# Performance work log

Hardware: AMD Instinct MI355X
Metric: run time of the kernel (lower is better)

Reference implementation:

```python
import jax, jax.numpy as jnp
import numpy as np

G = 29      # grid_size
D = 15      # displacement_width
R = 0.4     # disp_range
C = 16      # feature channels
S = 48      # feature spatial size
D3 = D ** 3


def _axis_coords(n, scale=1.0):
    # torch affine_grid (align_corners=False) coords: -1 + (2i+1)/n
    i = jnp.arange(n, dtype=jnp.float32)
    return scale * ((2.0 * i + 1.0) / n - 1.0)


def _make_grid(n, scale=1.0):
    # affine_grid flatten order is (d,h,w) with last dim (x,y,z)
    c = _axis_coords(n, scale)
    zz, yy, xx = jnp.meshgrid(c, c, c, indexing='ij')
    return jnp.stack([xx, yy, zz], axis=-1).reshape(-1, 3)  # [n^3, 3]


def _tri_sample(feat, pts):
    # feat [C,Dz,Hy,Wx]; pts [N,3] normalized (x,y,z); border-clamped trilinear
    Cc, Dz, Hy, Wx = feat.shape
    def unnorm(c, n):
        return jnp.clip(((c + 1.0) * n - 1.0) * 0.5, 0.0, n - 1.0)
    px = unnorm(pts[:, 0], Wx)
    py = unnorm(pts[:, 1], Hy)
    pz = unnorm(pts[:, 2], Dz)
    x0f, y0f, z0f = jnp.floor(px), jnp.floor(py), jnp.floor(pz)
    wx, wy, wz = px - x0f, py - y0f, pz - z0f
    x0 = x0f.astype(jnp.int32); y0 = y0f.astype(jnp.int32); z0 = z0f.astype(jnp.int32)
    x1 = jnp.minimum(x0 + 1, Wx - 1)
    y1 = jnp.minimum(y0 + 1, Hy - 1)
    z1 = jnp.minimum(z0 + 1, Dz - 1)
    flat = feat.reshape(Cc, -1)
    def g(zi, yi, xi):
        return flat[:, (zi * Hy + yi) * Wx + xi]  # [C,N]
    return (g(z0, y0, x0) * ((1 - wz) * (1 - wy) * (1 - wx))
          + g(z0, y0, x1) * ((1 - wz) * (1 - wy) * wx)
          + g(z0, y1, x0) * ((1 - wz) * wy * (1 - wx))
          + g(z0, y1, x1) * ((1 - wz) * wy * wx)
          + g(z1, y0, x0) * (wz * (1 - wy) * (1 - wx))
          + g(z1, y0, x1) * (wz * (1 - wy) * wx)
          + g(z1, y1, x0) * (wz * wy * (1 - wx))
          + g(z1, y1, x1) * (wz * wy * wx))


def _avg3(x):  # 3x3x3 avg pool, stride 1, VALID, over last 3 dims of [N,a,b,c]
    s = jax.lax.reduce_window(x, 0.0, jax.lax.add, (1, 3, 3, 3), (1, 1, 1, 1), 'VALID')
    return s / 27.0


def _min3(x):  # 3x3x3 min pool == -maxpool(-x)
    return jax.lax.reduce_window(x, float('inf'), jax.lax.min, (1, 3, 3, 3), (1, 1, 1, 1), 'VALID')


def _pad_rep(x, p):  # ReplicationPad3d over last 3 dims
    return jnp.pad(x, ((0, 0), (p, p), (p, p), (p, p)), mode='edge')


def _minavg_disp(x):  # pad1 -> min3 -> avg3 -> avg3  (size preserved)
    return _avg3(_avg3(_min3(_pad_rep(x, 3))))


def _avg_grid(x):  # pad2 -> avg3 -> avg3 (size preserved)
    return _avg3(_avg3(_pad_rep(x, 2)))


def setup_inputs() -> dict:
    key = jax.random.key(0)
    k1, k2 = jax.random.split(key)
    feat00 = jax.random.normal(k1, (1, C, S, S, S), dtype=jnp.float32)
    feat50 = jax.random.normal(k2, (1, C, S, S, S), dtype=jnp.float32)
    alpha = jnp.array([1.0, 0.1, 1.0, 1.0, 0.1, 1.0], dtype=jnp.float32)
    return {"feat00": feat00, "feat50": feat50, "alpha": alpha}


def reference(feat00, feat50, alpha):
    grid = _make_grid(G)        # [G^3,3]
    shift = _make_grid(D, R)    # [D^3,3]
    f0 = feat00[0]
    f5 = feat50[0]

    def slab(g):  # g [G^2,3] -> cost [G^2, D^3]
        pts = (g[:, None, :] + shift[None, :, :]).reshape(-1, 3)
        mov = _tri_sample(f5, pts).reshape(C, G * G, D3)
        fix = _tri_sample(f0, g)[:, :, None]            # [C,G^2,1]
        d = fix - mov
        return alpha[1] + alpha[0] * jnp.sum(d * d, axis=0)

    # scan over G slabs (as the torch loop does) to bound memory
    dc = jax.lax.map(jax.checkpoint(slab), grid.reshape(G, G * G, 3))
    dc = dc.reshape(G ** 3, D, D, D)                    # deeds_cost

    def disp_to_grid(x):
        return x.reshape(G ** 3, D3).T.reshape(D3, G, G, G)

    def grid_to_disp(x):
        return x.reshape(D3, G ** 3).T.reshape(G ** 3, D, D, D)

    c = _minavg_disp(dc)
    ca = grid_to_disp(_avg_grid(disp_to_grid(c)))
    c = alpha[4] + alpha[2] * dc + alpha[3] * ca
    c = _minavg_disp(c)
    ca2 = _avg_grid(disp_to_grid(c)).reshape(D3, G ** 3).T   # [G^3, D^3]
    cost_soft = jax.nn.softmax(-alpha[5] * ca2, axis=1)
    pred_xyz = cost_soft @ shift                              # [G^3, 3]
    return cost_soft, pred_xyz
```

## Files before the change

### kernel.cpp

```cpp
#include <hip/hip_runtime.h>
#include <cstdint>

#define GG   29
#define GG2  841
#define GG3  24389
#define DD   15
#define DD3  3375
#define SS   48
#define CC   16
#define NVOX (SS*SS*SS)
#define FT_ELEMS (NVOX*CC)
#define WXY  20
#define WZC  6
#define WELE4 (WXY*WXY*WZC)

#define MW0 (1.0f/9.0f)
#define MW1 (2.0f/9.0f)
#define MW2 (3.0f/9.0f)

__device__ __forceinline__ int clampi(int v, int lo, int hi) {
    return min(max(v, lo), hi);
}

__device__ __forceinline__ float4 f4min3(float4 a, float4 b, float4 c) {
    return make_float4(fminf(fminf(a.x,b.x),c.x), fminf(fminf(a.y,b.y),c.y),
                       fminf(fminf(a.z,b.z),c.z), fminf(fminf(a.w,b.w),c.w));
}
__device__ __forceinline__ void f4acc(float4& o, float w, float4 a) {
    o.x += w*a.x; o.y += w*a.y; o.z += w*a.z; o.w += w*a.w;
}

__global__ void __launch_bounds__(256) k_transpose4(const float* __restrict__ f,
                                                    float* __restrict__ ft) {
    int v = blockIdx.x * 256 + threadIdx.x;
    int cg4 = blockIdx.y;
    float4 o = make_float4(f[(4*cg4+0)*NVOX + v], f[(4*cg4+1)*NVOX + v],
                           f[(4*cg4+2)*NVOX + v], f[(4*cg4+3)*NVOX + v]);
    ((float4*)ft)[(size_t)cg4 * NVOX + v] = o;
}

template<int JZ0, int NJZ>
__device__ __forceinline__ void cost_chunk(const float4* __restrict__ f5f4,
                                           float4* win, const float4* fixs4,
                                           int tid, float pzb, int xb, int yb,
                                           int orel, float wx, float wy,
                                           bool active, float (&acc)[15]) {
    float pz0 = fminf(fmaxf(pzb + 1.28f * (float)JZ0, 0.0f), 47.0f);
    int zb = min((int)floorf(pz0), SS - WZC);
    int   z0r[NJZ];
    float wzs[NJZ];
    #pragma unroll
    for (int k = 0; k < NJZ; ++k) {
        float pz = fminf(fmaxf(pzb + 1.28f * (float)(JZ0 + k), 0.0f), 47.0f);
        int z0 = min((int)floorf(pz), 46);
        z0r[k] = z0 - zb;
        wzs[k] = pz - (float)z0;
    }

    int vox[10];
    #pragma unroll
    for (int k = 0; k < 10; ++k) {
        int idx = tid + (k << 8);
        if (idx < WELE4) {
            int lz  = idx / 400;
            int rem = idx - lz * 400;
            int ly  = rem / 20;
            int lx  = rem - ly * 20;
            vox[k] = ((zb + lz) * SS + (yb + ly)) * SS + (xb + lx);
        }
    }

    auto bilin = [&](int zr) -> float4 {
        const float4* P = win + zr * 400 + orel;
        float4 a = P[0], b = P[1], c = P[20], d = P[21];
        float r0x = a.x + wx*(b.x-a.x), r0y = a.y + wx*(b.y-a.y);
        float r0z = a.z + wx*(b.z-a.z), r0w = a.w + wx*(b.w-a.w);
        float r1x = c.x + wx*(d.x-c.x), r1y = c.y + wx*(d.y-c.y);
        float r1z = c.z + wx*(d.z-c.z), r1w = c.w + wx*(d.w-c.w);
        return make_float4(r0x + wy*(r1x-r0x), r0y + wy*(r1y-r0y),
                           r0z + wy*(r1z-r0z), r0w + wy*(r1w-r0w));
    };

    #pragma unroll 1
    for (int cg4 = 0; cg4 < 4; ++cg4) {
        const float4* src = f5f4 + (size_t)cg4 * NVOX;
        #pragma unroll
        for (int k = 0; k < 10; ++k) {
            int idx = tid + (k << 8);
            if (idx < WELE4) win[idx] = src[vox[k]];
        }
        __syncthreads();

        if (active) {
            float4 fx = fixs4[cg4];
            float4 pA = make_float4(0.f,0.f,0.f,0.f), pB = pA;
            int zprev = -99;
            #pragma unroll
            for (int k = 0; k < NJZ; ++k) {
                int zr = z0r[k]; float wz = wzs[k];
                if (zr != zprev) {
                    if (zr == zprev + 1) pA = pB;
                    else                 pA = bilin(zr);
                    pB = bilin(zr + 1);
                    zprev = zr;
                }
                float mx = pA.x + wz*(pB.x-pA.x);
                float my = pA.y + wz*(pB.y-pA.y);
                float mz = pA.z + wz*(pB.z-pA.z);
                float mw = pA.w + wz*(pB.w-pA.w);
                float dx = fx.x - mx, dy = fx.y - my, dz = fx.z - mz, dw = fx.w - mw;
                acc[JZ0 + k] += dx*dx + dy*dy + dz*dz + dw*dw;
            }
        }
        __syncthreads();
    }
}

__global__ void __launch_bounds__(256, 4) k_cost4(const float* __restrict__ f5t,
                                                  const float* __restrict__ feat00,
                                                  const float* __restrict__ alpha,
                                                  float* __restrict__ dc) {
    __shared__ float4 win[WELE4];
    __shared__ float4 fixs4[4];

    int tid = threadIdx.x;
    int g = blockIdx.x;
    int gx = g % GG; int gy = (g / GG) % GG; int gz = g / GG2;

    if (tid < CC) {
        int giv[3] = {gx, gy, gz};
        int i0[3]; float w[3];
        #pragma unroll
        for (int a = 0; a < 3; ++a) {
            float cgv = (2.0f * giv[a] + 1.0f) / 29.0f - 1.0f;
            float p = ((cgv + 1.0f) * 48.0f - 1.0f) * 0.5f;
            p = fminf(fmaxf(p, 0.0f), 47.0f);
            float fl = floorf(p);
            i0[a] = (int)fl; w[a] = p - fl;
        }
        int x0 = i0[0], y0 = i0[1], z0 = i0[2];
        int x1 = min(x0 + 1, 47), y1 = min(y0 + 1, 47), z1 = min(z0 + 1, 47);
        float wx = w[0], wy = w[1], wz = w[2];
        float ux = 1.0f - wx, uy = 1.0f - wy, uz = 1.0f - wz;
        const float* fc = feat00 + (size_t)tid * NVOX;
        int zy00 = (z0 * SS + y0) * SS, zy01 = (z0 * SS + y1) * SS;
        int zy10 = (z1 * SS + y0) * SS, zy11 = (z1 * SS + y1) * SS;
        ((float*)fixs4)[tid] =
              uz*uy*ux * fc[zy00 + x0] + uz*uy*wx * fc[zy00 + x1]
            + uz*wy*ux * fc[zy01 + x0] + uz*wy*wx * fc[zy01 + x1]
            + wz*uy*ux * fc[zy10 + x0] + wz*uy*wx * fc[zy10 + x1]
            + wz*wy*ux * fc[zy11 + x0] + wz*wy*wx * fc[zy11 + x1];
    }

    float pxb = 24.0f * (float)(2 * gx + 1) / 29.0f - 9.46f;
    float pyb = 24.0f * (float)(2 * gy + 1) / 29.0f - 9.46f;
    float pzb = 24.0f * (float)(2 * gz + 1) / 29.0f - 9.46f;
    int xb = min((int)floorf(fminf(fmaxf(pxb, 0.0f), 47.0f)), SS - WXY);
    int yb = min((int)floorf(fminf(fmaxf(pyb, 0.0f), 47.0f)), SS - WXY);

    bool active = tid < 225;
    int jx = tid % 15, jy = tid / 15;
    float px = fminf(fmaxf(pxb + 1.28f * (float)jx, 0.0f), 47.0f);
    float py = fminf(fmaxf(pyb + 1.28f * (float)jy, 0.0f), 47.0f);
    int x0 = min((int)floorf(px), 46);
    int y0 = min((int)floorf(py), 46);
    float wx = px - (float)x0;
    float wy = py - (float)y0;
    int orel = (y0 - yb) * WXY + (x0 - xb);

    float acc[15];
    #pragma unroll
    for (int k = 0; k < 15; ++k) acc[k] = 0.0f;

    const float4* f5f4 = (const float4*)f5t;
    cost_chunk<0, 4>(f5f4, win, fixs4, tid, pzb, xb, yb, orel, wx, wy, active, acc);
    cost_chunk<4, 4>(f5f4, win, fixs4, tid, pzb, xb, yb, orel, wx, wy, active, acc);
    cost_chunk<8, 4>(f5f4, win, fixs4, tid, pzb, xb, yb, orel, wx, wy, active, acc);
    cost_chunk<12,3>(f5f4, win, fixs4, tid, pzb, xb, yb, orel, wx, wy, active, acc);

    float a0 = alpha[0], a1 = alpha[1];
    if (active) {
        float* dcrow = dc + (size_t)g * DD3;
        #pragma unroll
        for (int k = 0; k < 15; ++k) dcrow[k * 225 + tid] = a1 + a0 * acc[k];
    }
}

__device__ __forceinline__ void minavg_cols(float* U, float* V, float (&v)[15],
                                            int tid, float* __restrict__ outrow) {
    if (tid < 225) {
        float m[20];
        #pragma unroll
        for (int zi = 0; zi < 20; ++zi)
            m[zi] = fminf(fminf(v[clampi(zi-3,0,14)], v[clampi(zi-2,0,14)]),
                          v[clampi(zi-1,0,14)]);
        float4* u4 = (float4*)&U[tid*20];
        const float4* m4 = (const float4*)m;
        #pragma unroll
        for (int q = 0; q < 5; ++q) u4[q] = m4[q];
    }
    __syncthreads();
    for (int c = tid; c < 285; c += 256) {
        int sx = c % 15, yi = c / 15;
        const float4* A = (const float4*)&U[(clampi(yi-3,0,14)*15 + sx)*20];
        const float4* B = (const float4*)&U[(clampi(yi-2,0,14)*15 + sx)*20];
        const float4* Cc= (const float4*)&U[(clampi(yi-1,0,14)*15 + sx)*20];
        float4* vv = (float4*)&V[c*20];
        #pragma unroll
        for (int q = 0; q < 5; ++q) vv[q] = f4min3(A[q], B[q], Cc[q]);
    }
    __syncthreads();
    for (int c = tid; c < 361; c += 256) {
        int xi = c % 19, yi = c / 19;
        int s0 = clampi(xi-3,0,14), s1 = clampi(xi-2,0,14), s2 = clampi(xi-1,0,14);
        const float4* A = (const float4*)&V[(yi*15 + s0)*20];
        const float4* B = (const float4*)&V[(yi*15 + s1)*20];
        const float4* Cc= (const float4*)&V[(yi*15 + s2)*20];
        float m[20];
        float4* m4 = (float4*)m;
        #pragma unroll
        for (int q = 0; q < 5; ++q) m4[q] = f4min3(A[q], B[q], Cc[q]);
        float cz[16];
        #pragma unroll
        for (int zi = 0; zi < 15; ++zi)
            cz[zi] = MW0*(m[zi] + m[zi+4]) + MW1*(m[zi+1] + m[zi+3]) + MW2*m[zi+2];
        cz[15] = cz[14];
        float4* u4 = (float4*)&U[c*16];
        const float4* c4 = (const float4*)cz;
        #pragma unroll
        for (int q = 0; q < 4; ++q) u4[q] = c4[q];
    }
    __syncthreads();
    for (int c = tid; c < 285; c += 256) {
        int xi = c % 19, yi = c / 19;
        float4 o0 = make_float4(0.f,0.f,0.f,0.f), o1 = o0, o2 = o0, o3 = o0;
        const float W[5] = {MW0, MW1, MW2, MW1, MW0};
        #pragma unroll
        for (int t = 0; t < 5; ++t) {
            const float4* A = (const float4*)&U[((yi+t)*19 + xi)*16];
            float w = W[t];
            f4acc(o0, w, A[0]); f4acc(o1, w, A[1]);
            f4acc(o2, w, A[2]); f4acc(o3, w, A[3]);
        }
        float4* vv = (float4*)&V[c*16];
        vv[0] = o0; vv[1] = o1; vv[2] = o2; vv[3] = o3;
    }
    __syncthreads();
    if (tid < 225) {
        int xi = tid % 15, yi = tid / 15;
        float4 o0 = make_float4(0.f,0.f,0.f,0.f), o1 = o0, o2 = o0, o3 = o0;
        const float W[5] = {MW0, MW1, MW2, MW1, MW0};
        #pragma unroll
        for (int t = 0; t < 5; ++t) {
            const float4* A = (const float4*)&V[(yi*19 + xi + t)*16];
            float w = W[t];
            f4acc(o0, w, A[0]); f4acc(o1, w, A[1]);
            f4acc(o2, w, A[2]); f4acc(o3, w, A[3]);
        }
        float4* u4 = (float4*)&U[tid*16];
        u4[0] = o0; u4[1] = o1; u4[2] = o2; u4[3] = o3;
    }
    __syncthreads();
    for (int d = tid; d < DD3; d += 256)
        outrow[d] = U[(d % 225)*16 + d/225];
}

__global__ void __launch_bounds__(256) k_minavg2(const float* __restrict__ in, float* out) {
    __shared__ __align__(16) float U[5776];
    __shared__ __align__(16) float V[5700];
    int tid = threadIdx.x;
    size_t base = (size_t)blockIdx.x * DD3;
    float v[15];
    if (tid < 225) {
        #pragma unroll
        for (int z = 0; z < 15; ++z) v[z] = in[base + z*225 + tid];
    }
    minavg_cols(U, V, v, tid, out + base);
}

__global__ void __launch_bounds__(256) k_conv_grid(const float* in, float* out, int axis) {
    int d = blockIdx.x * 256 + threadIdx.x;
    if (d >= DD3) return;
    int line = blockIdx.y;
    size_t base, step;
    if (axis == 0) { base = (size_t)line * GG * DD3; step = DD3; }
    else           { int gz = line / GG, gx = line % GG;
                     base = ((size_t)gz * GG2 + gx) * DD3; step = (size_t)GG * DD3; }
    base += (size_t)d;
    float v[GG];
    #pragma unroll
    for (int i = 0; i < GG; ++i) v[i] = in[base + (size_t)i * step];
    #pragma unroll
    for (int i = 0; i < GG; ++i) {
        int im2 = i-2 < 0 ? 0 : i-2, im1 = i-1 < 0 ? 0 : i-1;
        int ip2 = i+2 > 28 ? 28 : i+2, ip1 = i+1 > 28 ? 28 : i+1;
        out[base + (size_t)i * step] = MW0*(v[im2] + v[ip2]) + MW1*(v[im1] + v[ip1]) + MW2*v[i];
    }
}

__global__ void __launch_bounds__(256) k_zcomb2(const float* __restrict__ t2,
                                                const float* __restrict__ dcin,
                                                const float* __restrict__ alpha,
                                                float* c3out) {
    __shared__ __align__(16) float U[5776];
    __shared__ __align__(16) float V[5700];
    int tid = threadIdx.x;
    int g = blockIdx.x;
    int gx = g % GG; int gy = (g / GG) % GG; int gz = g / GG2;
    float a2 = alpha[2], a3 = alpha[3], a4 = alpha[4];
    size_t rb0 = ((size_t)((clampi(gz-2,0,28)*GG + gy)*GG + gx)) * DD3;
    size_t rb1 = ((size_t)((clampi(gz-1,0,28)*GG + gy)*GG + gx)) * DD3;
    size_t rb2 = ((size_t)((gz*GG + gy)*GG + gx)) * DD3;
    size_t rb3 = ((size_t)((clampi(gz+1,0,28)*GG + gy)*GG + gx)) * DD3;
    size_t rb4 = ((size_t)((clampi(gz+2,0,28)*GG + gy)*GG + gx)) * DD3;
    const float* drow = dcin + (size_t)g * DD3;
    float v[15];
    if (tid < 225) {
        #pragma unroll
        for (int z = 0; z < 15; ++z) {
            int d = z*225 + tid;
            float ca = MW0*(t2[rb0+d] + t2[rb4+d]) + MW1*(t2[rb1+d] + t2[rb3+d])
                     + MW2*t2[rb2+d];
            v[z] = a4 + a2 * drow[d] + a3 * ca;
        }
    }
    minavg_cols(U, V, v, tid, c3out + (size_t)g * DD3);
}

__global__ void __launch_bounds__(256) k_zsoftmax(const float* __restrict__ t4,
                                                  const float* __restrict__ alpha,
                                                  float* __restrict__ cost,
                                                  float* __restrict__ pred) {
    __shared__ float row[DD3];
    __shared__ float4 red4[256];
    int tid = threadIdx.x;
    int g = blockIdx.x;
    int gx = g % GG; int gy = (g / GG) % GG; int gz = g / GG2;
    float a5 = alpha[5];
    size_t rb0 = ((size_t)((clampi(gz-2,0,28)*GG + gy)*GG + gx)) * DD3;
    size_t rb1 = ((size_t)((clampi(gz-1,0,28)*GG + gy)*GG + gx)) * DD3;
    size_t rb2 = ((size_t)((gz*GG + gy)*GG + gx)) * DD3;
    size_t rb3 = ((size_t)((clampi(gz+1,0,28)*GG + gy)*GG + gx)) * DD3;
    size_t rb4 = ((size_t)((clampi(gz+2,0,28)*GG + gy)*GG + gx)) * DD3;

    float lmax = -3.0e38f;
    for (int d = tid; d < DD3; d += 256) {
        float ca = MW0*(t4[rb0+d] + t4[rb4+d]) + MW1*(t4[rb1+d] + t4[rb3+d]) + MW2*t4[rb2+d];
        float vv = -a5 * ca;
        row[d] = vv;
        lmax = fmaxf(lmax, vv);
    }
    red4[tid].x = lmax;
    __syncthreads();
    for (int s = 128; s > 0; s >>= 1) {
        if (tid < s) red4[tid].x = fmaxf(red4[tid].x, red4[tid + s].x);
        __syncthreads();
    }
    float m = red4[0].x;
    __syncthreads();

    float s0 = 0.f, s1 = 0.f, s2 = 0.f, s3 = 0.f;
    for (int d = tid; d < DD3; d += 256) {
        float p = expf(row[d] - m);
        row[d] = p;
        int jx = d % 15; int r = d / 15; int jy = r % 15; int jz = r / 15;
        s0 += p;
        s1 += p * (0.4f * ((2.0f * jx + 1.0f) / 15.0f - 1.0f));
        s2 += p * (0.4f * ((2.0f * jy + 1.0f) / 15.0f - 1.0f));
        s3 += p * (0.4f * ((2.0f * jz + 1.0f) / 15.0f - 1.0f));
    }
    red4[tid] = make_float4(s0, s1, s2, s3);
    __syncthreads();
    for (int s = 128; s > 0; s >>= 1) {
        if (tid < s) {
            float4 a = red4[tid], b = red4[tid + s];
            red4[tid] = make_float4(a.x + b.x, a.y + b.y, a.z + b.z, a.w + b.w);
        }
        __syncthreads();
    }
    float4 tot = red4[0];
    float inv = 1.0f / tot.x;
    size_t base = (size_t)g * DD3;
    for (int d = tid; d < DD3; d += 256) cost[base + d] = row[d] * inv;
    if (tid == 0) {
        pred[g*3 + 0] = tot.y * inv;
        pred[g*3 + 1] = tot.z * inv;
        pred[g*3 + 2] = tot.w * inv;
    }
}

extern "C" void kernel_launch(void* const* d_in, const int* in_sizes, int n_in,
                              void* d_out, int out_size, void* d_ws, size_t ws_size,
                              hipStream_t stream) {
    const float* feat00 = (const float*)d_in[0];
    const float* feat50 = (const float*)d_in[1];
    const float* alpha  = (const float*)d_in[2];
    float* out = (float*)d_out;
    float* ws  = (float*)d_ws;

    float* ft5  = ws;
    float* S0   = ws + FT_ELEMS;
    float* DOUT = out;
    float* pred = out + (size_t)GG3 * DD3;

    size_t need = ((size_t)FT_ELEMS + (size_t)GG3 * DD3) * sizeof(float);
    if (ws_size < need) return;

    k_transpose4<<<dim3(NVOX / 256, 4), 256, 0, stream>>>(feat50, ft5);

    k_cost4<<<GG3, 256, 0, stream>>>(ft5, feat00, alpha, S0);
    k_minavg2<<<GG3, 256, 0, stream>>>(S0, DOUT);
    dim3 cgrid((DD3 + 255) / 256, GG2);
    k_conv_grid<<<cgrid, 256, 0, stream>>>(DOUT, DOUT, 0);
    k_conv_grid<<<cgrid, 256, 0, stream>>>(DOUT, DOUT, 1);
    k_zcomb2<<<GG3, 256, 0, stream>>>(DOUT, S0, alpha, S0);
    k_conv_grid<<<cgrid, 256, 0, stream>>>(S0, S0, 0);
    k_conv_grid<<<cgrid, 256, 0, stream>>>(S0, S0, 1);
    k_zsoftmax<<<GG3, 256, 0, stream>>>(S0, alpha, out, pred);
}
```

Baseline: 2.812 ms.

## Fuse x/y grid smoothing passes into one LDS-tiled kernel and pad cost window rows

Two separate strided conv-over-grid passes (along x and y) become a single kernel per z-plane that loads an 841x8 displacement chunk into LDS, runs both 5-tap passes there, and writes the result back once. This halves the global round-trips for each smoothing stage and replaces wide-stride per-thread loads with short contiguous 32-byte segments. Separately, the cost kernel's shared window gets a row pitch of 21 instead of 20 to reduce LDS bank conflicts in the bilinear fetches. The risk is that the 8-wide chunks give short, poorly coalesced global accesses.

```diff
diff --git a/kernel.cpp b/kernel.cpp
--- a/kernel.cpp
+++ b/kernel.cpp
@@ -11,8 +11,12 @@
 #define NVOX (SS*SS*SS)
 #define FT_ELEMS (NVOX*CC)
 #define WXY  20
+#define WROW 21
 #define WZC  6
+#define WPL  (WROW*WXY)
 #define WELE4 (WXY*WXY*WZC)
+#define DCH  8
+#define NCH  ((DD3 + DCH - 1) / DCH)
 
 #define MW0 (1.0f/9.0f)
 #define MW1 (2.0f/9.0f)
@@ -58,6 +62,7 @@
     }
 
     int vox[10];
+    int ldsp[10];
     #pragma unroll
     for (int k = 0; k < 10; ++k) {
         int idx = tid + (k << 8);
@@ -66,13 +71,14 @@
             int rem = idx - lz * 400;
             int ly  = rem / 20;
             int lx  = rem - ly * 20;
-            vox[k] = ((zb + lz) * SS + (yb + ly)) * SS + (xb + lx);
+            vox[k]  = ((zb + lz) * SS + (yb + ly)) * SS + (xb + lx);
+            ldsp[k] = lz * WPL + ly * WROW + lx;
         }
     }
 
     auto bilin = [&](int zr) -> float4 {
-        const float4* P = win + zr * 400 + orel;
-        float4 a = P[0], b = P[1], c = P[20], d = P[21];
+        const float4* P = win + zr * WPL + orel;
+        float4 a = P[0], b = P[1], c = P[WROW], d = P[WROW+1];
         float r0x = a.x + wx*(b.x-a.x), r0y = a.y + wx*(b.y-a.y);
         float r0z = a.z + wx*(b.z-a.z), r0w = a.w + wx*(b.w-a.w);
         float r1x = c.x + wx*(d.x-c.x), r1y = c.y + wx*(d.y-c.y);
@@ -87,7 +93,7 @@
         #pragma unroll
         for (int k = 0; k < 10; ++k) {
             int idx = tid + (k << 8);
-            if (idx < WELE4) win[idx] = src[vox[k]];
+            if (idx < WELE4) win[ldsp[k]] = src[vox[k]];
         }
         __syncthreads();
 
@@ -116,11 +122,11 @@
     }
 }
 
-__global__ void __launch_bounds__(256, 4) k_cost4(const float* __restrict__ f5t,
+__global__ void __launch_bounds__(256, 4) k_cost5(const float* __restrict__ f5t,
                                                   const float* __restrict__ feat00,
                                                   const float* __restrict__ alpha,
                                                   float* __restrict__ dc) {
-    __shared__ float4 win[WELE4];
+    __shared__ float4 win[WPL * WZC];
     __shared__ float4 fixs4[4];
 
     int tid = threadIdx.x;
@@ -166,7 +172,7 @@
     int y0 = min((int)floorf(py), 46);
     float wx = px - (float)x0;
     float wy = py - (float)y0;
-    int orel = (y0 - yb) * WXY + (x0 - xb);
+    int orel = (y0 - yb) * WROW + (x0 - xb);
 
     float acc[15];
     #pragma unroll
@@ -278,23 +284,43 @@
     minavg_cols(U, V, v, tid, out + base);
 }
 
-__global__ void __launch_bounds__(256) k_conv_grid(const float* in, float* out, int axis) {
-    int d = blockIdx.x * 256 + threadIdx.x;
-    if (d >= DD3) return;
-    int line = blockIdx.y;
-    size_t base, step;
-    if (axis == 0) { base = (size_t)line * GG * DD3; step = DD3; }
-    else           { int gz = line / GG, gx = line % GG;
-                     base = ((size_t)gz * GG2 + gx) * DD3; step = (size_t)GG * DD3; }
-    base += (size_t)d;
-    float v[GG];
-    #pragma unroll
-    for (int i = 0; i < GG; ++i) v[i] = in[base + (size_t)i * step];
-    #pragma unroll
-    for (int i = 0; i < GG; ++i) {
-        int im2 = i-2 < 0 ? 0 : i-2, im1 = i-1 < 0 ? 0 : i-1;
-        int ip2 = i+2 > 28 ? 28 : i+2, ip1 = i+1 > 28 ? 28 : i+1;
-        out[base + (size_t)i * step] = MW0*(v[im2] + v[ip2]) + MW1*(v[im1] + v[ip1]) + MW2*v[i];
+__global__ void __launch_bounds__(256) k_convxy(const float* __restrict__ in,
+                                                float* __restrict__ out) {
+    __shared__ float T[GG2 * DCH];
+    __shared__ float X[GG2 * DCH];
+    int tid = threadIdx.x;
+    int chunk = blockIdx.x % NCH;
+    int gz    = blockIdx.x / NCH;
+    int d0 = chunk * DCH;
+    size_t pbase = (size_t)gz * GG2 * DD3 + d0;
+
+    for (int idx = tid; idx < GG2 * DCH; idx += 256) {
+        int dd = idx & (DCH-1), gp = idx >> 3;
+        int d = d0 + dd;
+        T[idx] = (d < DD3) ? in[pbase + (size_t)gp * DD3 + dd] : 0.0f;
+    }
+    __syncthreads();
+    for (int idx = tid; idx < GG2 * DCH; idx += 256) {
+        int dd = idx & (DCH-1), gp = idx >> 3;
+        int gx = gp % GG, gy = gp / GG;
+        int xm2 = gx-2 < 0 ? 0 : gx-2, xm1 = gx-1 < 0 ? 0 : gx-1;
+        int xp1 = gx+1 > 28 ? 28 : gx+1, xp2 = gx+2 > 28 ? 28 : gx+2;
+        int rb = gy * GG;
+        X[idx] = MW0*(T[(rb+xm2)*DCH+dd] + T[(rb+xp2)*DCH+dd])
+               + MW1*(T[(rb+xm1)*DCH+dd] + T[(rb+xp1)*DCH+dd])
+               + MW2* T[(rb+gx )*DCH+dd];
+    }
+    __syncthreads();
+    for (int idx = tid; idx < GG2 * DCH; idx += 256) {
+        int dd = idx & (DCH-1), gp = idx >> 3;
+        int gx = gp % GG, gy = gp / GG;
+        int ym2 = gy-2 < 0 ? 0 : gy-2, ym1 = gy-1 < 0 ? 0 : gy-1;
+        int yp1 = gy+1 > 28 ? 28 : gy+1, yp2 = gy+2 > 28 ? 28 : gy+2;
+        float vv = MW0*(X[(ym2*GG+gx)*DCH+dd] + X[(yp2*GG+gx)*DCH+dd])
+                 + MW1*(X[(ym1*GG+gx)*DCH+dd] + X[(yp1*GG+gx)*DCH+dd])
+                 + MW2* X[(gy *GG+gx)*DCH+dd];
+        int d = d0 + dd;
+        if (d < DD3) out[pbase + (size_t)gp * DD3 + dd] = vv;
     }
 }
 
@@ -408,13 +434,10 @@
 
     k_transpose4<<<dim3(NVOX / 256, 4), 256, 0, stream>>>(feat50, ft5);
 
-    k_cost4<<<GG3, 256, 0, stream>>>(ft5, feat00, alpha, S0);
+    k_cost5<<<GG3, 256, 0, stream>>>(ft5, feat00, alpha, S0);
     k_minavg2<<<GG3, 256, 0, stream>>>(S0, DOUT);
-    dim3 cgrid((DD3 + 255) / 256, GG2);
-    k_conv_grid<<<cgrid, 256, 0, stream>>>(DOUT, DOUT, 0);
-    k_conv_grid<<<cgrid, 256, 0, stream>>>(DOUT, DOUT, 1);
+    k_convxy<<<GG * NCH, 256, 0, stream>>>(DOUT, DOUT);
     k_zcomb2<<<GG3, 256, 0, stream>>>(DOUT, S0, alpha, S0);
-    k_conv_grid<<<cgrid, 256, 0, stream>>>(S0, S0, 0);
-    k_conv_grid<<<cgrid, 256, 0, stream>>>(S0, S0, 1);
+    k_convxy<<<GG * NCH, 256, 0, stream>>>(S0, S0);
     k_zsoftmax<<<GG3, 256, 0, stream>>>(S0, alpha, out, pred);
 }
```

New measurement: 3.824 ms. +36.0%, slower.

## Fuse x and y grid convolutions into one shared-memory tiled kernel

Applied to the files above, without the earlier changes.

Two separate passes of the 5-tap grid convolution along x and y become one kernel. Each block stages a z-plane of 841 grid points for 16 displacement channels in shared memory, applies both 1D filters in registers and writes back once. This halves global memory round-trips over the roughly 330 MB cost volume for each of the two smoothing stages. In exchange it uses larger shared memory per block (about 54 KB) and narrow 16-float contiguous accesses. It also leaves many threads idle, since only 29*16 of 512 threads compute.

```diff
diff --git a/kernel.cpp b/kernel.cpp
--- a/kernel.cpp
+++ b/kernel.cpp
@@ -13,6 +13,9 @@
 #define WXY  20
 #define WZC  6
 #define WELE4 (WXY*WXY*WZC)
+#define DCH16 16
+#define NCH16 211
+#define TST   843
 
 #define MW0 (1.0f/9.0f)
 #define MW1 (2.0f/9.0f)
@@ -278,23 +281,53 @@
     minavg_cols(U, V, v, tid, out + base);
 }
 
-__global__ void __launch_bounds__(256) k_conv_grid(const float* in, float* out, int axis) {
-    int d = blockIdx.x * 256 + threadIdx.x;
-    if (d >= DD3) return;
-    int line = blockIdx.y;
-    size_t base, step;
-    if (axis == 0) { base = (size_t)line * GG * DD3; step = DD3; }
-    else           { int gz = line / GG, gx = line % GG;
-                     base = ((size_t)gz * GG2 + gx) * DD3; step = (size_t)GG * DD3; }
-    base += (size_t)d;
-    float v[GG];
-    #pragma unroll
-    for (int i = 0; i < GG; ++i) v[i] = in[base + (size_t)i * step];
-    #pragma unroll
-    for (int i = 0; i < GG; ++i) {
-        int im2 = i-2 < 0 ? 0 : i-2, im1 = i-1 < 0 ? 0 : i-1;
-        int ip2 = i+2 > 28 ? 28 : i+2, ip1 = i+1 > 28 ? 28 : i+1;
-        out[base + (size_t)i * step] = MW0*(v[im2] + v[ip2]) + MW1*(v[im1] + v[ip1]) + MW2*v[i];
+__global__ void __launch_bounds__(512) k_convxy2(const float* __restrict__ in,
+                                                 float* __restrict__ out) {
+    __shared__ float T[DCH16 * TST];
+    int tid = threadIdx.x;
+    int chunk = blockIdx.x % NCH16;
+    int gz    = blockIdx.x / NCH16;
+    int d0 = chunk * DCH16;
+    int nv = min(DCH16, DD3 - d0);
+    size_t pbase = (size_t)gz * GG2 * DD3 + d0;
+
+    for (int idx = tid; idx < GG2 * DCH16; idx += 512) {
+        int gp = idx >> 4, dd = idx & 15;
+        if (dd < nv) T[dd * TST + gp] = in[pbase + (size_t)gp * DD3 + dd];
+    }
+    __syncthreads();
+
+    float o[29];
+    int cgx = -1, cdd = 0;
+    if (tid < 29 * nv) {
+        cgx = tid % 29; cdd = tid / 29;
+        const float* Tb = T + cdd * TST;
+        int xm2 = cgx-2 < 0 ? 0 : cgx-2, xm1 = cgx-1 < 0 ? 0 : cgx-1;
+        int xp1 = cgx+1 > 28 ? 28 : cgx+1, xp2 = cgx+2 > 28 ? 28 : cgx+2;
+        float X[29];
+        #pragma unroll
+        for (int j = 0; j < 29; ++j) {
+            int rb = j * 29;
+            X[j] = MW0*(Tb[rb+xm2] + Tb[rb+xp2]) + MW1*(Tb[rb+xm1] + Tb[rb+xp1])
+                 + MW2* Tb[rb+cgx];
+        }
+        #pragma unroll
+        for (int gy = 0; gy < 29; ++gy) {
+            int ym2 = gy-2 < 0 ? 0 : gy-2, ym1 = gy-1 < 0 ? 0 : gy-1;
+            int yp1 = gy+1 > 28 ? 28 : gy+1, yp2 = gy+2 > 28 ? 28 : gy+2;
+            o[gy] = MW0*(X[ym2] + X[yp2]) + MW1*(X[ym1] + X[yp1]) + MW2*X[gy];
+        }
+    }
+    __syncthreads();
+    if (cgx >= 0) {
+        float* Tb = T + cdd * TST;
+        #pragma unroll
+        for (int gy = 0; gy < 29; ++gy) Tb[gy * 29 + cgx] = o[gy];
+    }
+    __syncthreads();
+    for (int idx = tid; idx < GG2 * DCH16; idx += 512) {
+        int gp = idx >> 4, dd = idx & 15;
+        if (dd < nv) out[pbase + (size_t)gp * DD3 + dd] = T[dd * TST + gp];
     }
 }
 
@@ -410,11 +443,8 @@
 
     k_cost4<<<GG3, 256, 0, stream>>>(ft5, feat00, alpha, S0);
     k_minavg2<<<GG3, 256, 0, stream>>>(S0, DOUT);
-    dim3 cgrid((DD3 + 255) / 256, GG2);
-    k_conv_grid<<<cgrid, 256, 0, stream>>>(DOUT, DOUT, 0);
-    k_conv_grid<<<cgrid, 256, 0, stream>>>(DOUT, DOUT, 1);
+    k_convxy2<<<GG * NCH16, 512, 0, stream>>>(DOUT, DOUT);
     k_zcomb2<<<GG3, 256, 0, stream>>>(DOUT, S0, alpha, S0);
-    k_conv_grid<<<cgrid, 256, 0, stream>>>(S0, S0, 0);
-    k_conv_grid<<<cgrid, 256, 0, stream>>>(S0, S0, 1);
+    k_convxy2<<<GG * NCH16, 512, 0, stream>>>(S0, S0);
     k_zsoftmax<<<GG3, 256, 0, stream>>>(S0, alpha, out, pred);
 }
```

New measurement: 3.017 ms. +7.3%, slower.
